# Kernel tuning notes

Measured on AMD Instinct MI355X. Metric: run time of the kernel, lower is better.

Reference implementation:

```python
import jax, jax.numpy as jnp
import numpy as np

B, C, D_BB, D = 16384, 4, 2048, 512
MAX_NORM = 3.0
LN_EPS = 1e-5


def setup_inputs() -> dict:
    key = jax.random.key(0)
    ks = jax.random.split(key, 6)
    return {
        "thumbnails": jax.random.normal(ks[0], (B, C, D_BB), dtype=jnp.float32),
        # nn.Linear(backbone_dim, hidden_dim): weight [D, D_BB], bias [D]
        "proj_w": jax.random.normal(ks[1], (D, D_BB), dtype=jnp.float32) / np.float32(np.sqrt(D_BB)),
        "proj_b": jnp.zeros((D,), dtype=jnp.float32),
        # per-camera LayerNorm affine params [C, D]
        "gamma": jnp.ones((C, D), dtype=jnp.float32),
        "beta": jnp.zeros((C, D), dtype=jnp.float32),
        # per-camera SwiGLU weights (no bias), torch Linear convention [out, in]
        "w_gate": jax.random.normal(ks[2], (C, D, D), dtype=jnp.float32) / np.float32(np.sqrt(D)),
        "w_val": jax.random.normal(ks[3], (C, D, D), dtype=jnp.float32) / np.float32(np.sqrt(D)),
        # per-camera output proj D->36 (zero-init in module; small random for a useful baseline)
        "w_out": jax.random.normal(ks[4], (C, 36, D), dtype=jnp.float32) * np.float32(0.02),
    }


def _expm66(A):
    """Matrix exponential of [..., 6, 6] matrices with ||A||_F <= MAX_NORM.

    Scaling-and-squaring with a fixed order-12 Taylor series. After scaling by
    2^-4, ||A/16|| <= 0.1875, so the order-12 truncation error is << fp32 eps.
    Matches torch.linalg.matrix_exp to fp32 precision and is fully transposable.
    """
    s = 4  # number of squarings
    As = A * jnp.asarray(1.0 / (2 ** s), A.dtype)
    I = jnp.broadcast_to(jnp.eye(6, dtype=A.dtype), A.shape)
    E = I
    term = I
    for k in range(1, 13):
        term = jnp.matmul(term, As) * jnp.asarray(1.0 / k, A.dtype)
        E = E + term
    for _ in range(s):
        E = jnp.matmul(E, E)
    return E


def reference(thumbnails, proj_w, proj_b, gamma, beta, w_gate, w_val, w_out):
    # thumbnail projection: [B,C,D_BB] @ [D,D_BB]^T -> [B,C,D]
    reg = jnp.einsum('bce,de->bcd', thumbnails, proj_w) + proj_b
    # per-camera LayerNorm (biased variance, as in torch)
    mu = jnp.mean(reg, axis=-1, keepdims=True)
    var = jnp.var(reg, axis=-1, keepdims=True)
    xn = (reg - mu) * jax.lax.rsqrt(var + LN_EPS) * gamma + beta  # gamma/beta broadcast [C,D]
    # SwiGLU (per-camera weights)
    gate = jnp.einsum('bcd,cfd->bcf', xn, w_gate)
    val = jnp.einsum('bcd,cfd->bcf', xn, w_val)
    h = jax.nn.silu(gate) * val
    # project to Lie algebra, skew-symmetrize
    A = jnp.einsum('bcf,cof->bco', h, w_out).reshape(B, C, 6, 6)
    A = A - jnp.swapaxes(A, -1, -2)
    # Frobenius-norm clip to MAX_NORM
    frob = jnp.sqrt(jnp.sum(A * A, axis=(-2, -1), keepdims=True))
    A = A * (jnp.minimum(frob, MAX_NORM) / jnp.maximum(frob, 1e-8))
    # matrix exponential -> orthogonal deltaM, returned as [C, B, 6, 6]
    dM = _expm66(A)
    return jnp.swapaxes(dM, 0, 1)
```

## Files before the change

kernel.cpp:

```cpp
#include <hip/hip_runtime.h>
#include <cstdint>
#include <cstddef>


#define B_SZ   16384
#define C_CAM  4
#define DBB    2048
#define D_H    512

typedef __attribute__((ext_vector_type(8))) short  bf16x8;
typedef __attribute__((ext_vector_type(4))) float  f32x4;

__device__ __forceinline__ unsigned short f2b(float f) {
    union { float f; unsigned u; } v; v.f = f;
    unsigned r = (v.u + 0x7FFFu + ((v.u >> 16) & 1u)) >> 16;
    return (unsigned short)r;
}
__device__ __forceinline__ float b2f(unsigned short u) {
    union { unsigned u; float f; } v; v.u = ((unsigned)u) << 16;
    return v.f;
}

__global__ void k_cvt(const float* __restrict__ src, unsigned short* __restrict__ dst, int n) {
    int i = blockIdx.x * blockDim.x + threadIdx.x;
    int stride = gridDim.x * blockDim.x;
    for (; i < n; i += stride) dst[i] = f2b(src[i]);
}

__global__ void k_cvt_wout(const float* __restrict__ src, unsigned short* __restrict__ dst) {
    int i = blockIdx.x * blockDim.x + threadIdx.x;
    if (i >= C_CAM * 48 * D_H) return;
    int col = i & (D_H - 1);
    int row = (i >> 9) % 48;
    int c   = i / (48 * D_H);
    dst[i] = (row < 36) ? f2b(src[((size_t)c * 36 + row) * D_H + col]) : (unsigned short)0;
}

__global__ __launch_bounds__(256)
void k_proj(const float* __restrict__ A, const unsigned short* __restrict__ Bw,
            const float* __restrict__ bias, unsigned short* __restrict__ regb) {
    __shared__ unsigned short lsA[128 * 72];
    __shared__ unsigned short lsB[128 * 72];
    const int t = threadIdx.x;
    const int tile_n = blockIdx.x * 128;
    const int tile_m = blockIdx.y * 128;
    const int w = t >> 6, l = t & 63, lr = l & 15, quad = l >> 4;
    const int wm = (w >> 1) * 64, wn = (w & 1) * 64;

    f32x4 acc[4][4];
#pragma unroll
    for (int i = 0; i < 4; i++)
#pragma unroll
        for (int j = 0; j < 4; j++) acc[i][j] = (f32x4){0.f, 0.f, 0.f, 0.f};

    const int ar = t >> 4, ac = (t & 15) * 4;
    const int br = t >> 3, bc = (t & 7) * 8;

    for (int kt = 0; kt < DBB / 64; ++kt) {
        __syncthreads();
#pragma unroll
        for (int p = 0; p < 8; p++) {
            const int row = p * 16 + ar;
            const float4 v = *(const float4*)(A + (size_t)(tile_m + row) * DBB + kt * 64 + ac);
            unsigned p0 = (unsigned)f2b(v.x) | ((unsigned)f2b(v.y) << 16);
            unsigned p1 = (unsigned)f2b(v.z) | ((unsigned)f2b(v.w) << 16);
            *(uint2*)(&lsA[row * 72 + ac]) = make_uint2(p0, p1);
        }
#pragma unroll
        for (int p = 0; p < 4; p++) {
            const int row = p * 32 + br;
            *(uint4*)(&lsB[row * 72 + bc]) =
                *(const uint4*)(Bw + (size_t)(tile_n + row) * DBB + kt * 64 + bc);
        }
        __syncthreads();
#pragma unroll
        for (int kk = 0; kk < 2; ++kk) {
            bf16x8 af[4], bfr[4];
#pragma unroll
            for (int i = 0; i < 4; i++)
                af[i] = *(const bf16x8*)(&lsA[(wm + i * 16 + lr) * 72 + kk * 32 + quad * 8]);
#pragma unroll
            for (int j = 0; j < 4; j++)
                bfr[j] = *(const bf16x8*)(&lsB[(wn + j * 16 + lr) * 72 + kk * 32 + quad * 8]);
#pragma unroll
            for (int i = 0; i < 4; i++)
#pragma unroll
                for (int j = 0; j < 4; j++)
                    acc[i][j] = __builtin_amdgcn_mfma_f32_16x16x32_bf16(af[i], bfr[j], acc[i][j], 0, 0, 0);
        }
    }
#pragma unroll
    for (int j = 0; j < 4; j++) {
        const int col = tile_n + wn + j * 16 + lr;
        const float bv = bias[col];
#pragma unroll
        for (int i = 0; i < 4; i++)
#pragma unroll
            for (int r = 0; r < 4; r++) {
                const int row = tile_m + wm + i * 16 + quad * 4 + r;
                regb[(size_t)row * D_H + col] = f2b(acc[i][j][r] + bv);
            }
    }
}

__global__ __launch_bounds__(256)
void k_ln(const unsigned short* __restrict__ regb, const float* __restrict__ gamma,
          const float* __restrict__ beta, unsigned short* __restrict__ xnb) {
    const int t = threadIdx.x;
    const int wave = t >> 6, l = t & 63;
    const int r = blockIdx.x * 4 + wave;
    const int c = r & 3, b = r >> 2;

    const uint4 pk = *(const uint4*)(regb + (size_t)r * D_H + l * 8);
    const unsigned short* ps = (const unsigned short*)&pk;
    float x[8];
#pragma unroll
    for (int j = 0; j < 8; j++) x[j] = b2f(ps[j]);

    float s = 0.f, ss = 0.f;
#pragma unroll
    for (int j = 0; j < 8; j++) { s += x[j]; ss += x[j] * x[j]; }
#pragma unroll
    for (int off = 32; off > 0; off >>= 1) {
        s  += __shfl_xor(s, off);
        ss += __shfl_xor(ss, off);
    }
    const float mu  = s * (1.0f / 512.0f);
    const float var = ss * (1.0f / 512.0f) - mu * mu;
    const float rs  = rsqrtf(var + 1e-5f);

    unsigned short o[8];
#pragma unroll
    for (int j = 0; j < 8; j++) {
        const int d = l * 8 + j;
        o[j] = f2b((x[j] - mu) * rs * gamma[c * D_H + d] + beta[c * D_H + d]);
    }
    *(uint4*)(xnb + ((size_t)c * B_SZ + b) * D_H + l * 8) = *(const uint4*)o;
}

__global__ __launch_bounds__(256)
void k_swiglu(const unsigned short* __restrict__ xnb, const unsigned short* __restrict__ wg,
              const unsigned short* __restrict__ wv, unsigned short* __restrict__ hb) {
    __shared__ unsigned short lsA[128 * 72];
    __shared__ unsigned short lsG[128 * 72];
    __shared__ unsigned short lsV[128 * 72];
    const int t = threadIdx.x;
    const int tile_n = blockIdx.x * 128;
    const int tile_m = blockIdx.y * 128;
    const int cam = blockIdx.z;
    const unsigned short* Ac = xnb + (size_t)cam * B_SZ * D_H;
    const unsigned short* Gc = wg + (size_t)cam * D_H * D_H;
    const unsigned short* Vc = wv + (size_t)cam * D_H * D_H;
    const int w = t >> 6, l = t & 63, lr = l & 15, quad = l >> 4;
    const int wm = (w >> 1) * 64, wn = (w & 1) * 64;

    f32x4 ag[4][4], av[4][4];
#pragma unroll
    for (int i = 0; i < 4; i++)
#pragma unroll
        for (int j = 0; j < 4; j++) { ag[i][j] = (f32x4){0.f,0.f,0.f,0.f}; av[i][j] = (f32x4){0.f,0.f,0.f,0.f}; }

    const int br = t >> 3, bc = (t & 7) * 8;

    for (int kt = 0; kt < D_H / 64; ++kt) {
        __syncthreads();
#pragma unroll
        for (int p = 0; p < 4; p++) {
            const int row = p * 32 + br;
            *(uint4*)(&lsA[row * 72 + bc]) =
                *(const uint4*)(Ac + (size_t)(tile_m + row) * D_H + kt * 64 + bc);
            *(uint4*)(&lsG[row * 72 + bc]) =
                *(const uint4*)(Gc + (size_t)(tile_n + row) * D_H + kt * 64 + bc);
            *(uint4*)(&lsV[row * 72 + bc]) =
                *(const uint4*)(Vc + (size_t)(tile_n + row) * D_H + kt * 64 + bc);
        }
        __syncthreads();
#pragma unroll
        for (int kk = 0; kk < 2; ++kk) {
            bf16x8 af[4];
#pragma unroll
            for (int i = 0; i < 4; i++)
                af[i] = *(const bf16x8*)(&lsA[(wm + i * 16 + lr) * 72 + kk * 32 + quad * 8]);
#pragma unroll
            for (int j = 0; j < 4; j++) {
                bf16x8 gf = *(const bf16x8*)(&lsG[(wn + j * 16 + lr) * 72 + kk * 32 + quad * 8]);
                bf16x8 vf = *(const bf16x8*)(&lsV[(wn + j * 16 + lr) * 72 + kk * 32 + quad * 8]);
#pragma unroll
                for (int i = 0; i < 4; i++) {
                    ag[i][j] = __builtin_amdgcn_mfma_f32_16x16x32_bf16(af[i], gf, ag[i][j], 0, 0, 0);
                    av[i][j] = __builtin_amdgcn_mfma_f32_16x16x32_bf16(af[i], vf, av[i][j], 0, 0, 0);
                }
            }
        }
    }
#pragma unroll
    for (int i = 0; i < 4; i++)
#pragma unroll
        for (int j = 0; j < 4; j++)
#pragma unroll
            for (int r = 0; r < 4; r++) {
                const int row = tile_m + wm + i * 16 + quad * 4 + r;
                const int col = tile_n + wn + j * 16 + lr;
                const float g = ag[i][j][r], v = av[i][j][r];
                const float h = g * v / (1.0f + __expf(-g));
                hb[((size_t)cam * B_SZ + row) * D_H + col] = f2b(h);
            }
}

__global__ __launch_bounds__(256)
void k_outproj(const unsigned short* __restrict__ hb, const unsigned short* __restrict__ wo,
               float* __restrict__ Abuf) {
    __shared__ unsigned short lsA[128 * 72];
    __shared__ unsigned short lsB[48 * 72];
    const int t = threadIdx.x;
    const int tile_m = blockIdx.y * 128;
    const int cam = blockIdx.z;
    const unsigned short* Ac = hb + (size_t)cam * B_SZ * D_H;
    const unsigned short* Bc = wo + (size_t)cam * 48 * D_H;
    const int w = t >> 6, l = t & 63, lr = l & 15, quad = l >> 4;

    f32x4 acc[2][3];
#pragma unroll
    for (int i = 0; i < 2; i++)
#pragma unroll
        for (int j = 0; j < 3; j++) acc[i][j] = (f32x4){0.f,0.f,0.f,0.f};

    const int br = t >> 3, bc = (t & 7) * 8;

    for (int kt = 0; kt < D_H / 64; ++kt) {
        __syncthreads();
#pragma unroll
        for (int p = 0; p < 4; p++) {
            const int row = p * 32 + br;
            *(uint4*)(&lsA[row * 72 + bc]) =
                *(const uint4*)(Ac + (size_t)(tile_m + row) * D_H + kt * 64 + bc);
        }
#pragma unroll
        for (int p = 0; p < 2; p++) {
            const int flat = (p * 256 + t) * 8;
            if (flat < 48 * 64) {
                const int row = flat >> 6, col = flat & 63;
                *(uint4*)(&lsB[row * 72 + col]) =
                    *(const uint4*)(Bc + (size_t)row * D_H + kt * 64 + col);
            }
        }
        __syncthreads();
#pragma unroll
        for (int kk = 0; kk < 2; ++kk) {
            bf16x8 af[2], bfr[3];
#pragma unroll
            for (int i = 0; i < 2; i++)
                af[i] = *(const bf16x8*)(&lsA[(w * 32 + i * 16 + lr) * 72 + kk * 32 + quad * 8]);
#pragma unroll
            for (int j = 0; j < 3; j++)
                bfr[j] = *(const bf16x8*)(&lsB[(j * 16 + lr) * 72 + kk * 32 + quad * 8]);
#pragma unroll
            for (int i = 0; i < 2; i++)
#pragma unroll
                for (int j = 0; j < 3; j++)
                    acc[i][j] = __builtin_amdgcn_mfma_f32_16x16x32_bf16(af[i], bfr[j], acc[i][j], 0, 0, 0);
        }
    }
#pragma unroll
    for (int i = 0; i < 2; i++)
#pragma unroll
        for (int j = 0; j < 3; j++)
#pragma unroll
            for (int r = 0; r < 4; r++) {
                const int col = j * 16 + lr;
                if (col < 36) {
                    const int row = tile_m + w * 32 + i * 16 + quad * 4 + r;
                    Abuf[((size_t)cam * B_SZ + row) * 36 + col] = acc[i][j][r];
                }
            }
}

__global__ __launch_bounds__(128)
void k_expm(const float* __restrict__ Abuf, float* __restrict__ out) {
    const int gid = blockIdx.x * blockDim.x + threadIdx.x;
    if (gid >= B_SZ * C_CAM) return;
    const float* Ap = Abuf + (size_t)gid * 36;

    float a[36];
#pragma unroll
    for (int i = 0; i < 36; i++) a[i] = Ap[i];

    float S[36];
#pragma unroll
    for (int i = 0; i < 6; i++)
#pragma unroll
        for (int j = 0; j < 6; j++) S[i * 6 + j] = a[i * 6 + j] - a[j * 6 + i];

    float fr2 = 0.f;
#pragma unroll
    for (int i = 0; i < 36; i++) fr2 += S[i] * S[i];
    const float fr = sqrtf(fr2);
    const float sc = fminf(fr, 3.0f) / fmaxf(fr, 1e-8f) * 0.0625f;

    float As[36];
#pragma unroll
    for (int i = 0; i < 36; i++) As[i] = S[i] * sc;

    float E[36], T[36], tmp[36];
#pragma unroll
    for (int i = 0; i < 36; i++) { E[i] = (i % 7 == 0) ? 1.f : 0.f; T[i] = E[i]; }

#pragma unroll
    for (int k = 1; k <= 12; k++) {
        const float invk = 1.0f / (float)k;
#pragma unroll
        for (int i = 0; i < 6; i++)
#pragma unroll
            for (int j = 0; j < 6; j++) {
                float sum = 0.f;
#pragma unroll
                for (int q = 0; q < 6; q++) sum += T[i * 6 + q] * As[q * 6 + j];
                tmp[i * 6 + j] = sum * invk;
            }
#pragma unroll
        for (int i = 0; i < 36; i++) { T[i] = tmp[i]; E[i] += tmp[i]; }
    }
#pragma unroll
    for (int sq = 0; sq < 4; sq++) {
#pragma unroll
        for (int i = 0; i < 6; i++)
#pragma unroll
            for (int j = 0; j < 6; j++) {
                float sum = 0.f;
#pragma unroll
                for (int q = 0; q < 6; q++) sum += E[i * 6 + q] * E[q * 6 + j];
                tmp[i * 6 + j] = sum;
            }
#pragma unroll
        for (int i = 0; i < 36; i++) E[i] = tmp[i];
    }

    float* op = out + (size_t)gid * 36;
#pragma unroll
    for (int i = 0; i < 36; i++) op[i] = E[i];
}

extern "C" void kernel_launch(void* const* d_in, const int* in_sizes, int n_in,
                              void* d_out, int out_size, void* d_ws, size_t ws_size,
                              hipStream_t stream) {
    const float* thumb  = (const float*)d_in[0];
    const float* proj_w = (const float*)d_in[1];
    const float* proj_b = (const float*)d_in[2];
    const float* gamma  = (const float*)d_in[3];
    const float* beta   = (const float*)d_in[4];
    const float* w_gate = (const float*)d_in[5];
    const float* w_val  = (const float*)d_in[6];
    const float* w_out  = (const float*)d_in[7];

    char* ws = (char*)d_ws;
    unsigned short* regb = (unsigned short*)(ws + 0);
    unsigned short* xnb  = (unsigned short*)(ws + 67108864);
    unsigned short* hb   = (unsigned short*)(ws + 0);
    float*          Abuf = (float*)(ws + 67108864);
    unsigned short* pwb  = (unsigned short*)(ws + 134217728);
    unsigned short* wgb  = (unsigned short*)(ws + 136314880);
    unsigned short* wvb  = (unsigned short*)(ws + 138412032);
    unsigned short* wob  = (unsigned short*)(ws + 140509184);

    hipLaunchKernelGGL(k_cvt, dim3(1024), dim3(256), 0, stream, proj_w, pwb, D_H * DBB);
    hipLaunchKernelGGL(k_cvt, dim3(1024), dim3(256), 0, stream, w_gate, wgb, C_CAM * D_H * D_H);
    hipLaunchKernelGGL(k_cvt, dim3(1024), dim3(256), 0, stream, w_val, wvb, C_CAM * D_H * D_H);
    hipLaunchKernelGGL(k_cvt_wout, dim3((C_CAM * 48 * D_H + 255) / 256), dim3(256), 0, stream, w_out, wob);

    hipLaunchKernelGGL(k_proj, dim3(4, 512), dim3(256), 0, stream, thumb, pwb, proj_b, regb);
    hipLaunchKernelGGL(k_ln, dim3(B_SZ * C_CAM / 4), dim3(256), 0, stream, regb, gamma, beta, xnb);
    hipLaunchKernelGGL(k_swiglu, dim3(4, 128, 4), dim3(256), 0, stream, xnb, wgb, wvb, hb);
    hipLaunchKernelGGL(k_outproj, dim3(1, 128, 4), dim3(256), 0, stream, hb, wob, Abuf);
    hipLaunchKernelGGL(k_expm, dim3(B_SZ * C_CAM / 128), dim3(128), 0, stream, Abuf, (float*)d_out);
}
```

Baseline: 1.304 ms.

## Pre-convert thumbnails to bf16 and stage GEMM tiles via direct global-to-LDS loads

Adds a vectorized pass that converts the fp32 thumbnail activations to bf16 in workspace, so the projection GEMM can read bf16 operands. That GEMM, plus the SwiGLU and output-projection GEMMs, now fill shared memory with global_load_lds (direct global-to-LDS, no register round trip) using unpadded 32-wide K tiles. The goal is to cut register pressure and load instructions in the GEMM main loops. In exchange it adds an extra full-size pass over the thumbnails, needs a much larger workspace (the old path stays as a fallback), and the unpadded LDS layout may cause bank conflicts and twice as many barriers per K.

```diff
diff --git a/kernel.cpp b/kernel.cpp
--- a/kernel.cpp
+++ b/kernel.cpp
@@ -21,10 +21,25 @@
     return v.f;
 }
 
+#define GLDS(g, l) __builtin_amdgcn_global_load_lds( \
+    (const __attribute__((address_space(1))) unsigned int*)(g), \
+    (__attribute__((address_space(3))) unsigned int*)(l), 16, 0, 0)
+
 __global__ void k_cvt(const float* __restrict__ src, unsigned short* __restrict__ dst, int n) {
     int i = blockIdx.x * blockDim.x + threadIdx.x;
     int stride = gridDim.x * blockDim.x;
     for (; i < n; i += stride) dst[i] = f2b(src[i]);
+}
+
+__global__ __launch_bounds__(256)
+void k_cvt8(const float* __restrict__ src, unsigned short* __restrict__ dst, long n8) {
+    long i = (long)blockIdx.x * blockDim.x + threadIdx.x;
+    if (i >= n8) return;
+    const float4 a = ((const float4*)src)[i * 2];
+    const float4 b = ((const float4*)src)[i * 2 + 1];
+    unsigned short o[8] = {f2b(a.x), f2b(a.y), f2b(a.z), f2b(a.w),
+                           f2b(b.x), f2b(b.y), f2b(b.z), f2b(b.w)};
+    ((uint4*)dst)[i] = *(const uint4*)o;
 }
 
 __global__ void k_cvt_wout(const float* __restrict__ src, unsigned short* __restrict__ dst) {
@@ -37,8 +52,65 @@
 }
 
 __global__ __launch_bounds__(256)
-void k_proj(const float* __restrict__ A, const unsigned short* __restrict__ Bw,
-            const float* __restrict__ bias, unsigned short* __restrict__ regb) {
+void k_projb(const unsigned short* __restrict__ A, const unsigned short* __restrict__ Bw,
+             const float* __restrict__ bias, unsigned short* __restrict__ regb) {
+    __shared__ unsigned short lsA[128 * 32];
+    __shared__ unsigned short lsB[128 * 32];
+    const int t = threadIdx.x;
+    const int tile_n = blockIdx.x * 128;
+    const int tile_m = blockIdx.y * 128;
+    const int w = t >> 6, l = t & 63, lr = l & 15, quad = l >> 4;
+    const int wm = (w >> 1) * 64, wn = (w & 1) * 64;
+
+    f32x4 acc[4][4];
+#pragma unroll
+    for (int i = 0; i < 4; i++)
+#pragma unroll
+        for (int j = 0; j < 4; j++) acc[i][j] = (f32x4){0.f, 0.f, 0.f, 0.f};
+
+    const int srow = l >> 2, scol = (l & 3) * 8;
+    const unsigned short* baseA = A  + (size_t)(tile_m + w * 32 + srow) * DBB + scol;
+    const unsigned short* baseB = Bw + (size_t)(tile_n + w * 32 + srow) * DBB + scol;
+    unsigned short* ldsAw = &lsA[w * 32 * 32];
+    unsigned short* ldsBw = &lsB[w * 32 * 32];
+
+    for (int kt = 0; kt < DBB / 32; ++kt) {
+        __syncthreads();
+        GLDS(baseA + kt * 32,            ldsAw);
+        GLDS(baseA + kt * 32 + 16 * DBB, ldsAw + 16 * 32);
+        GLDS(baseB + kt * 32,            ldsBw);
+        GLDS(baseB + kt * 32 + 16 * DBB, ldsBw + 16 * 32);
+        __syncthreads();
+        bf16x8 af[4], bfr[4];
+#pragma unroll
+        for (int i = 0; i < 4; i++)
+            af[i] = *(const bf16x8*)(&lsA[(wm + i * 16 + lr) * 32 + quad * 8]);
+#pragma unroll
+        for (int j = 0; j < 4; j++)
+            bfr[j] = *(const bf16x8*)(&lsB[(wn + j * 16 + lr) * 32 + quad * 8]);
+#pragma unroll
+        for (int i = 0; i < 4; i++)
+#pragma unroll
+            for (int j = 0; j < 4; j++)
+                acc[i][j] = __builtin_amdgcn_mfma_f32_16x16x32_bf16(af[i], bfr[j], acc[i][j], 0, 0, 0);
+    }
+#pragma unroll
+    for (int j = 0; j < 4; j++) {
+        const int col = tile_n + wn + j * 16 + lr;
+        const float bv = bias[col];
+#pragma unroll
+        for (int i = 0; i < 4; i++)
+#pragma unroll
+            for (int r = 0; r < 4; r++) {
+                const int row = tile_m + wm + i * 16 + quad * 4 + r;
+                regb[(size_t)row * D_H + col] = f2b(acc[i][j][r] + bv);
+            }
+    }
+}
+
+__global__ __launch_bounds__(256)
+void k_projf(const float* __restrict__ A, const unsigned short* __restrict__ Bw,
+             const float* __restrict__ bias, unsigned short* __restrict__ regb) {
     __shared__ unsigned short lsA[128 * 72];
     __shared__ unsigned short lsB[128 * 72];
     const int t = threadIdx.x;
@@ -141,9 +213,9 @@
 __global__ __launch_bounds__(256)
 void k_swiglu(const unsigned short* __restrict__ xnb, const unsigned short* __restrict__ wg,
               const unsigned short* __restrict__ wv, unsigned short* __restrict__ hb) {
-    __shared__ unsigned short lsA[128 * 72];
-    __shared__ unsigned short lsG[128 * 72];
-    __shared__ unsigned short lsV[128 * 72];
+    __shared__ unsigned short lsA[128 * 32];
+    __shared__ unsigned short lsG[128 * 32];
+    __shared__ unsigned short lsV[128 * 32];
     const int t = threadIdx.x;
     const int tile_n = blockIdx.x * 128;
     const int tile_m = blockIdx.y * 128;
@@ -160,36 +232,35 @@
 #pragma unroll
         for (int j = 0; j < 4; j++) { ag[i][j] = (f32x4){0.f,0.f,0.f,0.f}; av[i][j] = (f32x4){0.f,0.f,0.f,0.f}; }
 
-    const int br = t >> 3, bc = (t & 7) * 8;
-
-    for (int kt = 0; kt < D_H / 64; ++kt) {
-        __syncthreads();
-#pragma unroll
-        for (int p = 0; p < 4; p++) {
-            const int row = p * 32 + br;
-            *(uint4*)(&lsA[row * 72 + bc]) =
-                *(const uint4*)(Ac + (size_t)(tile_m + row) * D_H + kt * 64 + bc);
-            *(uint4*)(&lsG[row * 72 + bc]) =
-                *(const uint4*)(Gc + (size_t)(tile_n + row) * D_H + kt * 64 + bc);
-            *(uint4*)(&lsV[row * 72 + bc]) =
-                *(const uint4*)(Vc + (size_t)(tile_n + row) * D_H + kt * 64 + bc);
-        }
-        __syncthreads();
-#pragma unroll
-        for (int kk = 0; kk < 2; ++kk) {
-            bf16x8 af[4];
-#pragma unroll
-            for (int i = 0; i < 4; i++)
-                af[i] = *(const bf16x8*)(&lsA[(wm + i * 16 + lr) * 72 + kk * 32 + quad * 8]);
-#pragma unroll
-            for (int j = 0; j < 4; j++) {
-                bf16x8 gf = *(const bf16x8*)(&lsG[(wn + j * 16 + lr) * 72 + kk * 32 + quad * 8]);
-                bf16x8 vf = *(const bf16x8*)(&lsV[(wn + j * 16 + lr) * 72 + kk * 32 + quad * 8]);
-#pragma unroll
-                for (int i = 0; i < 4; i++) {
-                    ag[i][j] = __builtin_amdgcn_mfma_f32_16x16x32_bf16(af[i], gf, ag[i][j], 0, 0, 0);
-                    av[i][j] = __builtin_amdgcn_mfma_f32_16x16x32_bf16(af[i], vf, av[i][j], 0, 0, 0);
-                }
+    const int srow = l >> 2, scol = (l & 3) * 8;
+    const unsigned short* baseA = Ac + (size_t)(tile_m + w * 32 + srow) * D_H + scol;
+    const unsigned short* baseG = Gc + (size_t)(tile_n + w * 32 + srow) * D_H + scol;
+    const unsigned short* baseV = Vc + (size_t)(tile_n + w * 32 + srow) * D_H + scol;
+    unsigned short* ldsAw = &lsA[w * 32 * 32];
+    unsigned short* ldsGw = &lsG[w * 32 * 32];
+    unsigned short* ldsVw = &lsV[w * 32 * 32];
+
+    for (int kt = 0; kt < D_H / 32; ++kt) {
+        __syncthreads();
+        GLDS(baseA + kt * 32,            ldsAw);
+        GLDS(baseA + kt * 32 + 16 * D_H, ldsAw + 16 * 32);
+        GLDS(baseG + kt * 32,            ldsGw);
+        GLDS(baseG + kt * 32 + 16 * D_H, ldsGw + 16 * 32);
+        GLDS(baseV + kt * 32,            ldsVw);
+        GLDS(baseV + kt * 32 + 16 * D_H, ldsVw + 16 * 32);
+        __syncthreads();
+        bf16x8 af[4];
+#pragma unroll
+        for (int i = 0; i < 4; i++)
+            af[i] = *(const bf16x8*)(&lsA[(wm + i * 16 + lr) * 32 + quad * 8]);
+#pragma unroll
+        for (int j = 0; j < 4; j++) {
+            bf16x8 gf = *(const bf16x8*)(&lsG[(wn + j * 16 + lr) * 32 + quad * 8]);
+            bf16x8 vf = *(const bf16x8*)(&lsV[(wn + j * 16 + lr) * 32 + quad * 8]);
+#pragma unroll
+            for (int i = 0; i < 4; i++) {
+                ag[i][j] = __builtin_amdgcn_mfma_f32_16x16x32_bf16(af[i], gf, ag[i][j], 0, 0, 0);
+                av[i][j] = __builtin_amdgcn_mfma_f32_16x16x32_bf16(af[i], vf, av[i][j], 0, 0, 0);
             }
         }
     }
@@ -210,14 +281,15 @@
 __global__ __launch_bounds__(256)
 void k_outproj(const unsigned short* __restrict__ hb, const unsigned short* __restrict__ wo,
                float* __restrict__ Abuf) {
-    __shared__ unsigned short lsA[128 * 72];
-    __shared__ unsigned short lsB[48 * 72];
+    __shared__ unsigned short lsA[128 * 32];
+    __shared__ unsigned short lsB[48 * 32];
     const int t = threadIdx.x;
     const int tile_m = blockIdx.y * 128;
     const int cam = blockIdx.z;
     const unsigned short* Ac = hb + (size_t)cam * B_SZ * D_H;
     const unsigned short* Bc = wo + (size_t)cam * 48 * D_H;
     const int w = t >> 6, l = t & 63, lr = l & 15, quad = l >> 4;
+    const int srow = l >> 2, scol = (l & 3) * 8;
 
     f32x4 acc[2][3];
 #pragma unroll
@@ -225,41 +297,29 @@
 #pragma unroll
         for (int j = 0; j < 3; j++) acc[i][j] = (f32x4){0.f,0.f,0.f,0.f};
 
-    const int br = t >> 3, bc = (t & 7) * 8;
-
-    for (int kt = 0; kt < D_H / 64; ++kt) {
-        __syncthreads();
-#pragma unroll
-        for (int p = 0; p < 4; p++) {
-            const int row = p * 32 + br;
-            *(uint4*)(&lsA[row * 72 + bc]) =
-                *(const uint4*)(Ac + (size_t)(tile_m + row) * D_H + kt * 64 + bc);
-        }
-#pragma unroll
-        for (int p = 0; p < 2; p++) {
-            const int flat = (p * 256 + t) * 8;
-            if (flat < 48 * 64) {
-                const int row = flat >> 6, col = flat & 63;
-                *(uint4*)(&lsB[row * 72 + col]) =
-                    *(const uint4*)(Bc + (size_t)row * D_H + kt * 64 + col);
-            }
-        }
-        __syncthreads();
-#pragma unroll
-        for (int kk = 0; kk < 2; ++kk) {
-            bf16x8 af[2], bfr[3];
-#pragma unroll
-            for (int i = 0; i < 2; i++)
-                af[i] = *(const bf16x8*)(&lsA[(w * 32 + i * 16 + lr) * 72 + kk * 32 + quad * 8]);
+    const unsigned short* baseA = Ac + (size_t)(tile_m + w * 32 + srow) * D_H + scol;
+    const unsigned short* baseB = Bc + (size_t)(w * 16 + srow) * D_H + scol;
+    unsigned short* ldsAw = &lsA[w * 32 * 32];
+    unsigned short* ldsBw = &lsB[w * 16 * 32];
+
+    for (int kt = 0; kt < D_H / 32; ++kt) {
+        __syncthreads();
+        GLDS(baseA + kt * 32,            ldsAw);
+        GLDS(baseA + kt * 32 + 16 * D_H, ldsAw + 16 * 32);
+        if (w < 3) GLDS(baseB + kt * 32, ldsBw);
+        __syncthreads();
+        bf16x8 af[2], bfr[3];
+#pragma unroll
+        for (int i = 0; i < 2; i++)
+            af[i] = *(const bf16x8*)(&lsA[(w * 32 + i * 16 + lr) * 32 + quad * 8]);
+#pragma unroll
+        for (int j = 0; j < 3; j++)
+            bfr[j] = *(const bf16x8*)(&lsB[(j * 16 + lr) * 32 + quad * 8]);
+#pragma unroll
+        for (int i = 0; i < 2; i++)
 #pragma unroll
             for (int j = 0; j < 3; j++)
-                bfr[j] = *(const bf16x8*)(&lsB[(j * 16 + lr) * 72 + kk * 32 + quad * 8]);
-#pragma unroll
-            for (int i = 0; i < 2; i++)
-#pragma unroll
-                for (int j = 0; j < 3; j++)
-                    acc[i][j] = __builtin_amdgcn_mfma_f32_16x16x32_bf16(af[i], bfr[j], acc[i][j], 0, 0, 0);
-        }
+                acc[i][j] = __builtin_amdgcn_mfma_f32_16x16x32_bf16(af[i], bfr[j], acc[i][j], 0, 0, 0);
     }
 #pragma unroll
     for (int i = 0; i < 2; i++)
@@ -353,23 +413,50 @@
     const float* w_out  = (const float*)d_in[7];
 
     char* ws = (char*)d_ws;
-    unsigned short* regb = (unsigned short*)(ws + 0);
-    unsigned short* xnb  = (unsigned short*)(ws + 67108864);
-    unsigned short* hb   = (unsigned short*)(ws + 0);
-    float*          Abuf = (float*)(ws + 67108864);
-    unsigned short* pwb  = (unsigned short*)(ws + 134217728);
-    unsigned short* wgb  = (unsigned short*)(ws + 136314880);
-    unsigned short* wvb  = (unsigned short*)(ws + 138412032);
-    unsigned short* wob  = (unsigned short*)(ws + 140509184);
-
-    hipLaunchKernelGGL(k_cvt, dim3(1024), dim3(256), 0, stream, proj_w, pwb, D_H * DBB);
-    hipLaunchKernelGGL(k_cvt, dim3(1024), dim3(256), 0, stream, w_gate, wgb, C_CAM * D_H * D_H);
-    hipLaunchKernelGGL(k_cvt, dim3(1024), dim3(256), 0, stream, w_val, wvb, C_CAM * D_H * D_H);
-    hipLaunchKernelGGL(k_cvt_wout, dim3((C_CAM * 48 * D_H + 255) / 256), dim3(256), 0, stream, w_out, wob);
-
-    hipLaunchKernelGGL(k_proj, dim3(4, 512), dim3(256), 0, stream, thumb, pwb, proj_b, regb);
-    hipLaunchKernelGGL(k_ln, dim3(B_SZ * C_CAM / 4), dim3(256), 0, stream, regb, gamma, beta, xnb);
-    hipLaunchKernelGGL(k_swiglu, dim3(4, 128, 4), dim3(256), 0, stream, xnb, wgb, wvb, hb);
-    hipLaunchKernelGGL(k_outproj, dim3(1, 128, 4), dim3(256), 0, stream, hb, wob, Abuf);
-    hipLaunchKernelGGL(k_expm, dim3(B_SZ * C_CAM / 128), dim3(128), 0, stream, Abuf, (float*)d_out);
-}
+    const size_t FAST_WS = 409141248ULL;
+
+    if (ws_size >= FAST_WS) {
+        unsigned short* Abf  = (unsigned short*)(ws);
+        unsigned short* regb = (unsigned short*)(ws + 268435456);
+        unsigned short* xnb  = (unsigned short*)(ws + 335544320);
+        unsigned short* hb   = (unsigned short*)(ws);
+        float*          Abuf = (float*)(ws + 268435456);
+        unsigned short* pwb  = (unsigned short*)(ws + 402653184);
+        unsigned short* wgb  = (unsigned short*)(ws + 404750336);
+        unsigned short* wvb  = (unsigned short*)(ws + 406847488);
+        unsigned short* wob  = (unsigned short*)(ws + 408944640);
+
+        hipLaunchKernelGGL(k_cvt8, dim3(65536), dim3(256), 0, stream,
+                           thumb, Abf, (long)B_SZ * C_CAM * DBB / 8);
+        hipLaunchKernelGGL(k_cvt, dim3(1024), dim3(256), 0, stream, proj_w, pwb, D_H * DBB);
+        hipLaunchKernelGGL(k_cvt, dim3(1024), dim3(256), 0, stream, w_gate, wgb, C_CAM * D_H * D_H);
+        hipLaunchKernelGGL(k_cvt, dim3(1024), dim3(256), 0, stream, w_val, wvb, C_CAM * D_H * D_H);
+        hipLaunchKernelGGL(k_cvt_wout, dim3((C_CAM * 48 * D_H + 255) / 256), dim3(256), 0, stream, w_out, wob);
+
+        hipLaunchKernelGGL(k_projb, dim3(4, 512), dim3(256), 0, stream, Abf, pwb, proj_b, regb);
+        hipLaunchKernelGGL(k_ln, dim3(B_SZ * C_CAM / 4), dim3(256), 0, stream, regb, gamma, beta, xnb);
+        hipLaunchKernelGGL(k_swiglu, dim3(4, 128, 4), dim3(256), 0, stream, xnb, wgb, wvb, hb);
+        hipLaunchKernelGGL(k_outproj, dim3(1, 128, 4), dim3(256), 0, stream, hb, wob, Abuf);
+        hipLaunchKernelGGL(k_expm, dim3(B_SZ * C_CAM / 128), dim3(128), 0, stream, Abuf, (float*)d_out);
+    } else {
+        unsigned short* regb = (unsigned short*)(ws + 0);
+        unsigned short* xnb  = (unsigned short*)(ws + 67108864);
+        unsigned short* hb   = (unsigned short*)(ws + 0);
+        float*          Abuf = (float*)(ws + 67108864);
+        unsigned short* pwb  = (unsigned short*)(ws + 134217728);
+        unsigned short* wgb  = (unsigned short*)(ws + 136314880);
+        unsigned short* wvb  = (unsigned short*)(ws + 138412032);
+        unsigned short* wob  = (unsigned short*)(ws + 140509184);
+
+        hipLaunchKernelGGL(k_cvt, dim3(1024), dim3(256), 0, stream, proj_w, pwb, D_H * DBB);
+        hipLaunchKernelGGL(k_cvt, dim3(1024), dim3(256), 0, stream, w_gate, wgb, C_CAM * D_H * D_H);
+        hipLaunchKernelGGL(k_cvt, dim3(1024), dim3(256), 0, stream, w_val, wvb, C_CAM * D_H * D_H);
+        hipLaunchKernelGGL(k_cvt_wout, dim3((C_CAM * 48 * D_H + 255) / 256), dim3(256), 0, stream, w_out, wob);
+
+        hipLaunchKernelGGL(k_projf, dim3(4, 512), dim3(256), 0, stream, thumb, pwb, proj_b, regb);
+        hipLaunchKernelGGL(k_ln, dim3(B_SZ * C_CAM / 4), dim3(256), 0, stream, regb, gamma, beta, xnb);
+        hipLaunchKernelGGL(k_swiglu, dim3(4, 128, 4), dim3(256), 0, stream, xnb, wgb, wvb, hb);
+        hipLaunchKernelGGL(k_outproj, dim3(1, 128, 4), dim3(256), 0, stream, hb, wob, Abuf);
+        hipLaunchKernelGGL(k_expm, dim3(B_SZ * C_CAM / 128), dim3(128), 0, stream, Abuf, (float*)d_out);
+    }
+}
```

Measured after the change: 1.183 ms. 9.3% less time.
